# Kernel optimization log

Hardware: AMD Instinct MI355X
Metric: run time of the kernel (lower is better)

The kernel has to match this reference:

```python
import jax, jax.numpy as jnp
import numpy as np

V, BLK, D, H, L = 50257, 2048, 768, 12, 4
HD = D // H
EPS = 1e-5


def _ln(x, w, b):
    mu = jnp.mean(x, axis=-1, keepdims=True)
    var = jnp.mean(jnp.square(x - mu), axis=-1, keepdims=True)
    return (x - mu) * jax.lax.rsqrt(var + EPS) * w + b


def setup_inputs() -> dict:
    key = jax.random.key(0)
    ks = iter(jax.random.split(key, 32))
    s = 0.02
    idx = jax.random.randint(next(ks), (2, 2048), 0, V)
    inp = {
        "idx": idx,
        "wte": jax.random.normal(next(ks), (V, D), jnp.float32) * s,
        "wpe": jax.random.normal(next(ks), (BLK, D), jnp.float32) * s,
        # stacked per-layer params [L, ...]
        "ln1_w": jnp.ones((L, D), jnp.float32),
        "ln1_b": jnp.zeros((L, D), jnp.float32),
        "attn_w": jax.random.normal(next(ks), (L, D, 3 * D), jnp.float32) * s,
        "attn_b": jnp.zeros((L, 3 * D), jnp.float32),
        "proj_w": jax.random.normal(next(ks), (L, D, D), jnp.float32) * (s / np.sqrt(2 * L)),
        "proj_b": jnp.zeros((L, D), jnp.float32),
        "ln2_w": jnp.ones((L, D), jnp.float32),
        "ln2_b": jnp.zeros((L, D), jnp.float32),
        "fc_w": jax.random.normal(next(ks), (L, D, 4 * D), jnp.float32) * s,
        "fc_b": jnp.zeros((L, 4 * D), jnp.float32),
        "fcp_w": jax.random.normal(next(ks), (L, 4 * D, D), jnp.float32) * (s / np.sqrt(2 * L)),
        "fcp_b": jnp.zeros((L, D), jnp.float32),
        "lnf_w": jnp.ones((D,), jnp.float32),
        "lnf_b": jnp.zeros((D,), jnp.float32),
    }
    return inp


def _gpt_forward(idx, wte, wpe, ln1_w, ln1_b, attn_w, attn_b, proj_w, proj_b,
                 ln2_w, ln2_b, fc_w, fc_b, fcp_w, fcp_b, lnf_w, lnf_b):
    B, T = idx.shape
    x = wte[idx] + wpe[:T]  # [B,T,D]; dropout p=0 -> identity
    causal = jnp.tril(jnp.ones((T, T), bool))
    scale = 1.0 / np.sqrt(HD)

    def block(x, p):
        l1w, l1b, aw, ab, pw, pb, l2w, l2b, fw, fb, fpw, fpb = p
        h = _ln(x, l1w, l1b)
        qkv = h @ aw + ab  # [B,T,3D]
        q, k, v = jnp.split(qkv, 3, axis=-1)
        q = q.reshape(B, T, H, HD).transpose(0, 2, 1, 3)  # [B,H,T,hd]
        k = k.reshape(B, T, H, HD).transpose(0, 2, 1, 3)
        v = v.reshape(B, T, H, HD).transpose(0, 2, 1, 3)
        att = jnp.einsum('bhqd,bhkd->bhqk', q, k) * scale
        att = jnp.where(causal, att, -jnp.inf)
        att = jax.nn.softmax(att, axis=-1)
        y = jnp.einsum('bhqk,bhkd->bhqd', att, v)
        y = y.transpose(0, 2, 1, 3).reshape(B, T, D)
        x = x + y @ pw + pb
        h2 = _ln(x, l2w, l2b)
        m = jax.nn.gelu(h2 @ fw + fb, approximate=False) @ fpw + fpb
        return x + m, None

    params = (ln1_w, ln1_b, attn_w, attn_b, proj_w, proj_b,
              ln2_w, ln2_b, fc_w, fc_b, fcp_w, fcp_b)
    x, _ = jax.lax.scan(block, x, params)
    x = _ln(x, lnf_w, lnf_b)
    # inference path: logits only for last position, lm_head tied to wte
    logits = x[:, -1:, :] @ wte.T  # [B,1,V]
    return logits


def reference(idx, wte, wpe, ln1_w, ln1_b, attn_w, attn_b, proj_w, proj_b,
              ln2_w, ln2_b, fc_w, fc_b, fcp_w, fcp_b, lnf_w, lnf_b):
    return _gpt_forward(idx, wte, wpe, ln1_w, ln1_b, attn_w, attn_b, proj_w, proj_b,
                        ln2_w, ln2_b, fc_w, fc_b, fcp_w, fcp_b, lnf_w, lnf_b)
```

## Files before the change

### kernel.cpp

```cpp
#include <hip/hip_runtime.h>
#include <math.h>

#define V 50257
#define B 2
#define T 2048
#define D 768
#define H 12
#define HD 64
#define L 4
#define D3 (3*D)
#define D4 (4*D)
#define NTOK (B*T)
#define EPS 1e-5f

typedef __bf16 v8bf __attribute__((ext_vector_type(8)));
typedef __bf16 v4bf __attribute__((ext_vector_type(4)));
typedef unsigned short v8us __attribute__((ext_vector_type(8)));
typedef float  v4f  __attribute__((ext_vector_type(4)));

#define GAS(p) ((const __attribute__((address_space(1))) void*)(p))
#define LAS(p) ((__attribute__((address_space(3))) void*)(p))

#define LIDX(row, chunk) ((row)*64 + ((((chunk) ^ ((row)&7)))<<3))
#define C2IDX(row, chunk) ((row)*256 + ((((chunk) ^ (((row)&7)<<2)))<<3))

#define SBAR() asm volatile("s_barrier" ::: "memory")

__device__ __forceinline__ float gelu_fast(float x) {
    float z  = fabsf(x) * 0.70710678118f;
    float tt = 1.f / (1.f + 0.3275911f * z);
    float poly = tt * (0.254829592f + tt * (-0.284496736f + tt * (1.421413741f +
                 tt * (-1.453152027f + tt * 1.061405429f))));
    float er = 1.f - poly * __expf(-z * z);
    er = (x < 0.f) ? -er : er;
    return 0.5f * x * (1.f + er);
}

__global__ __launch_bounds__(256) void prep_kernel(
        const int* __restrict__ idx, const float* __restrict__ wte,
        const float* __restrict__ wpe, float* __restrict__ x,
        const float* __restrict__ aw_all,  const float* __restrict__ pw_all,
        const float* __restrict__ fw_all,  const float* __restrict__ fpw_all,
        __bf16* __restrict__ awt_all, __bf16* __restrict__ pwt_all,
        __bf16* __restrict__ fwt_all, __bf16* __restrict__ fpwt_all) {
    int bid = blockIdx.x;
    if (bid < 3072) {
        int e = (bid * 256 + threadIdx.x) * 4;
        int pos = e / D;
        int d   = e - pos * D;
        int t   = pos & (T - 1);
        int tok = idx[pos];
        const float4 a  = *(const float4*)(wte + (size_t)tok * D + d);
        const float4 p4 = *(const float4*)(wpe + (size_t)t * D + d);
        float4 r; r.x = a.x + p4.x; r.y = a.y + p4.y; r.z = a.z + p4.z; r.w = a.w + p4.w;
        *(float4*)(x + e) = r;
        return;
    }
    bid -= 3072;
    const int l = bid / 6912; bid -= l * 6912;
    const float* W; __bf16* Wt; int K, N, bx, by;
    if (bid < 1728)      {             W = aw_all  + (size_t)l * D  * D3; Wt = awt_all  + (size_t)l * D3 * D;  K = D;  N = D3; bx = bid % 72; by = bid / 72; }
    else if (bid < 2304) { bid -= 1728; W = pw_all  + (size_t)l * D  * D;  Wt = pwt_all  + (size_t)l * D  * D;  K = D;  N = D;  bx = bid % 24; by = bid / 24; }
    else if (bid < 4608) { bid -= 2304; W = fw_all  + (size_t)l * D  * D4; Wt = fwt_all  + (size_t)l * D4 * D;  K = D;  N = D4; bx = bid % 96; by = bid / 96; }
    else                 { bid -= 4608; W = fpw_all + (size_t)l * D4 * D;  Wt = fpwt_all + (size_t)l * D  * D4; K = D4; N = D;  bx = bid % 24; by = bid / 24; }
    __shared__ float t[32][33];
    const int n0 = bx * 32, k0 = by * 32;
    const int tx = threadIdx.x & 31, ty = threadIdx.x >> 5;
    #pragma unroll
    for (int p = 0; p < 4; ++p)
        t[ty + 8 * p][tx] = W[(size_t)(k0 + ty + 8 * p) * N + n0 + tx];
    __syncthreads();
    #pragma unroll
    for (int p = 0; p < 4; ++p)
        Wt[(size_t)(n0 + ty + 8 * p) * K + k0 + tx] = (__bf16)t[tx][ty + 8 * p];
}

__global__ __launch_bounds__(256) void ln_kernel(const float* __restrict__ X,
                                                 const float* __restrict__ w,
                                                 const float* __restrict__ b,
                                                 __bf16* __restrict__ Y,
                                                 int src_mul, int src_off) {
    int srow = blockIdx.x * src_mul + src_off;
    const float* xr = X + (size_t)srow * D;
    float v[3];
    float s = 0.f, s2 = 0.f;
    #pragma unroll
    for (int j = 0; j < 3; ++j) {
        v[j] = xr[threadIdx.x + 256 * j];
        s += v[j];
        s2 += v[j] * v[j];
    }
    #pragma unroll
    for (int off = 32; off; off >>= 1) {
        s  += __shfl_xor(s, off);
        s2 += __shfl_xor(s2, off);
    }
    __shared__ float ss[4], ss2[4];
    int wave = threadIdx.x >> 6, lane = threadIdx.x & 63;
    if (lane == 0) { ss[wave] = s; ss2[wave] = s2; }
    __syncthreads();
    s  = ss[0] + ss[1] + ss[2] + ss[3];
    s2 = ss2[0] + ss2[1] + ss2[2] + ss2[3];
    float mu  = s * (1.f / D);
    float var = s2 * (1.f / D) - mu * mu;
    float rs  = rsqrtf(var + EPS);
    __bf16* yr = Y + (size_t)blockIdx.x * D;
    #pragma unroll
    for (int j = 0; j < 3; ++j) {
        int c = threadIdx.x + 256 * j;
        yr[c] = (__bf16)((v[j] - mu) * rs * w[c] + b[c]);
    }
}

template<bool DOGELU>
__global__ __launch_bounds__(512) void gemm256(const __bf16* __restrict__ A,
                                               const __bf16* __restrict__ Wt,
                                               const float* __restrict__ bias,
                                               __bf16* __restrict__ Cout,
                                               int N, int K) {
    __shared__ __align__(16) __bf16 sm[32768];
    const int tid  = threadIdx.x;
    const int w    = tid >> 6;
    const int lane = tid & 63;
    const int wm   = w >> 2;
    const int wn   = w & 3;

    int fid = blockIdx.y * gridDim.x + blockIdx.x;
    const int nwg = gridDim.x * gridDim.y;
    fid = (fid & 7) * (nwg >> 3) + (fid >> 3);
    const int row0 = (fid / gridDim.x) * 256;
    const int col0 = (fid % gridDim.x) * 256;

    const int l15 = lane & 15;
    const int lq8 = (lane >> 4) * 8;
    const __bf16* gAsrc[2];
    const __bf16* gBsrc[2];
    {
        #pragma unroll
        for (int rep = 0; rep < 2; ++rep) {
            int ga = w * 2 + rep;
            int awm = ga >> 3, ai = ga & 7;
            gAsrc[rep] = A + (size_t)(row0 + awm * 128 + ai * 16 + l15) * K + lq8;
            int gb = w * 2 + rep;
            int bwn = gb >> 2, bj = gb & 3;
            gBsrc[rep] = Wt + (size_t)(col0 + bwn * 64 + bj * 16 + l15) * K + lq8;
        }
    }

    auto stage = [&](int bsel) {
        __bf16* dst = sm + bsel * 16384;
        #pragma unroll
        for (int rep = 0; rep < 2; ++rep) {
            const int g = w * 2 + rep;
            __builtin_amdgcn_global_load_lds(GAS(gAsrc[rep]), LAS(dst + (size_t)(g * 64 + lane) * 8), 16, 0, 0);
            __builtin_amdgcn_global_load_lds(GAS(gBsrc[rep]), LAS(dst + 8192 + (size_t)(g * 64 + lane) * 8), 16, 0, 0);
            gAsrc[rep] += 32; gBsrc[rep] += 32;
        }
    };

    const int nt = K >> 5;
    stage(0);

    v4f acc[8][4] = {};
    for (int t = 0; t < nt; ++t) {
        const int cb = (t & 1) * 16384;
        if (t + 1 < nt) {
            stage((t + 1) & 1);
            asm volatile("s_waitcnt vmcnt(4)\n\ts_barrier" ::: "memory");
        } else {
            asm volatile("s_waitcnt vmcnt(0)\n\ts_barrier" ::: "memory");
        }
        v8bf bf[4];
        #pragma unroll
        for (int j = 0; j < 4; ++j)
            bf[j] = *(const v8bf*)(sm + cb + 8192 + (size_t)((wn * 4 + j) * 64 + lane) * 8);
        #pragma unroll
        for (int i = 0; i < 8; ++i) {
            v8bf af = *(const v8bf*)(sm + cb + (size_t)((wm * 8 + i) * 64 + lane) * 8);
            #pragma unroll
            for (int j = 0; j < 4; ++j)
                acc[i][j] = __builtin_amdgcn_mfma_f32_16x16x32_bf16(af, bf[j], acc[i][j], 0, 0, 0);
        }
        SBAR();
    }

    const int er = (lane >> 4) * 4;
    const int ec = lane & 15;
    #pragma unroll
    for (int half = 0; half < 2; ++half) {
        if (wm == half) {
            #pragma unroll
            for (int j = 0; j < 4; ++j) {
                const int col = wn * 64 + j * 16 + ec;
                const float bval = bias[col0 + col];
                const int chunk = col >> 3, ce = col & 7;
                #pragma unroll
                for (int i = 0; i < 8; ++i) {
                    const int rowb = i * 16 + er;
                    #pragma unroll
                    for (int rr = 0; rr < 4; ++rr) {
                        float vv = acc[i][j][rr] + bval;
                        if (DOGELU) vv = gelu_fast(vv);
                        sm[C2IDX(rowb + rr, chunk) + ce] = (__bf16)vv;
                    }
                }
            }
        }
        __syncthreads();
        #pragma unroll
        for (int c = 0; c < 8; ++c) {
            const int chunkid = tid + c * 512;
            const int row = chunkid >> 5;
            const int cc  = chunkid & 31;
            *(v8us*)(void*)(Cout + (size_t)(row0 + half * 128 + row) * N + col0 + cc * 8) =
                *(const v8us*)(const void*)(sm + C2IDX(row, cc));
        }
        __syncthreads();
    }
}

__global__ __launch_bounds__(256) void gemm64(const __bf16* __restrict__ A,
                                              const __bf16* __restrict__ Wt,
                                              const float* __restrict__ bias,
                                              const float* __restrict__ res,
                                              float* __restrict__ Cout,
                                              int N, int K) {
    __shared__ __align__(16) __bf16 sm[24576];
    const int tid  = threadIdx.x;
    const int w    = tid >> 6;
    const int lane = tid & 63;

    int fid = blockIdx.y * gridDim.x + blockIdx.x;
    const int nwg = gridDim.x * gridDim.y;
    fid = (fid & 7) * (nwg >> 3) + (fid >> 3);
    const int row0 = (fid / gridDim.x) * 64;
    const int col0 = (fid % gridDim.x) * 64;

    const int srow = ((tid >> 7) & 3) * 16 + (tid & 15);
    const int sk   = ((tid >> 4) & 7) * 8;
    const __bf16* gA0 = A  + (size_t)(row0 + srow) * K + sk;
    const __bf16* gA1 = gA0 + (size_t)32 * K;
    const __bf16* gB0 = Wt + (size_t)(col0 + srow) * K + sk;
    const __bf16* gB1 = gB0 + (size_t)32 * K;

    auto stage = [&](int bsel) {
        __bf16* dst = sm + bsel * 8192;
        __builtin_amdgcn_global_load_lds(GAS(gA0), LAS(dst + (size_t)tid * 8), 16, 0, 0);
        __builtin_amdgcn_global_load_lds(GAS(gA1), LAS(dst + (size_t)(tid + 256) * 8), 16, 0, 0);
        __builtin_amdgcn_global_load_lds(GAS(gB0), LAS(dst + 4096 + (size_t)tid * 8), 16, 0, 0);
        __builtin_amdgcn_global_load_lds(GAS(gB1), LAS(dst + 4096 + (size_t)(tid + 256) * 8), 16, 0, 0);
        gA0 += 64; gA1 += 64; gB0 += 64; gB1 += 64;
    };

    const int wr = w >> 1, wc = w & 1;
    const __bf16* rA = sm + wr * 2048 + lane * 8;
    const __bf16* rB = sm + 4096 + wc * 2048 + lane * 8;

    const int nt = K >> 6;
    stage(0); stage(1);

    v4f acc[2][2] = {};
    for (int t = 0; t < nt; ++t) {
        const int cb = (t % 3) * 8192;
        if (t + 2 < nt) {
            stage((t + 2) % 3);
            asm volatile("s_waitcnt vmcnt(8)\n\ts_barrier" ::: "memory");
        } else if (t + 1 < nt) {
            asm volatile("s_waitcnt vmcnt(4)\n\ts_barrier" ::: "memory");
        } else {
            asm volatile("s_waitcnt vmcnt(0)\n\ts_barrier" ::: "memory");
        }
        #pragma unroll
        for (int h = 0; h < 2; ++h) {
            v8bf af[2], bfr[2];
            #pragma unroll
            for (int i = 0; i < 2; ++i) af[i]  = *(const v8bf*)(rA + cb + i * 1024 + h * 512);
            #pragma unroll
            for (int j = 0; j < 2; ++j) bfr[j] = *(const v8bf*)(rB + cb + j * 1024 + h * 512);
            #pragma unroll
            for (int i = 0; i < 2; ++i)
                #pragma unroll
                for (int j = 0; j < 2; ++j)
                    acc[i][j] = __builtin_amdgcn_mfma_f32_16x16x32_bf16(af[i], bfr[j], acc[i][j], 0, 0, 0);
        }
        SBAR();
    }

    float* smf = (float*)sm;
    const int er = (lane >> 4) * 4;
    const int ec = lane & 15;
    #pragma unroll
    for (int j = 0; j < 2; ++j) {
        const int col = wc * 32 + j * 16 + ec;
        const float bval = bias[col0 + col];
        #pragma unroll
        for (int i = 0; i < 2; ++i) {
            #pragma unroll
            for (int rr = 0; rr < 4; ++rr) {
                const int row = wr * 32 + i * 16 + er + rr;
                smf[row * 64 + (col ^ ((row & 3) << 4))] = acc[i][j][rr] + bval;
            }
        }
    }
    __syncthreads();
    #pragma unroll
    for (int c = 0; c < 4; ++c) {
        const int chunkid = tid + c * 256;
        const int row = chunkid >> 4;
        const int c0  = (chunkid & 15) * 4;
        float4 vv = *(const float4*)(smf + row * 64 + (c0 ^ ((row & 3) << 4)));
        const float4 rv = *(const float4*)(res + (size_t)(row0 + row) * N + col0 + c0);
        vv.x += rv.x; vv.y += rv.y; vv.z += rv.z; vv.w += rv.w;
        *(float4*)(Cout + (size_t)(row0 + row) * N + col0 + c0) = vv;
    }
}

__global__ __launch_bounds__(256) void attn_mfma(const __bf16* __restrict__ qkv,
                                                 __bf16* __restrict__ y) {
    __shared__ __align__(16) __bf16 Qs[4096];
    __shared__ __align__(16) __bf16 Ks[4096];
    __shared__ __align__(16) __bf16 Vt[4096];
    __shared__ __align__(16) __bf16 Ps[4][1024];

    const int tid  = threadIdx.x;
    const int w    = tid >> 6;
    const int lane = tid & 63;
    const int quad = lane >> 4;
    const int l4   = lane & 15;

    int fid = blockIdx.x;
    const int nwg = gridDim.x;
    fid = (fid & 7) * (nwg >> 3) + (fid >> 3);

    const int qt = 31 - (fid & 31);
    const int bh = fid >> 5;
    const int b  = bh / H;
    const int h  = bh - b * H;
    const int q0 = qt * 64;

    const __bf16* base = qkv + (size_t)(b * T) * D3 + h * HD;

    {
        int c = tid;
        #pragma unroll
        for (int rep = 0; rep < 2; ++rep, c += 256) {
            int row = c >> 3, ch = c & 7;
            v8us v = *(const v8us*)(const void*)(base + (size_t)(q0 + row) * D3 + ch * 8);
            *(v8us*)(void*)(Qs + LIDX(row, ch)) = v;
        }
    }

    const int krow = tid >> 3, kch = tid & 7;
    const int vkp = tid & 31, vdc = tid >> 5;
    const __bf16* kp0 = base + D     + (size_t)krow * D3 + kch * 8;
    const __bf16* kp1 = kp0 + (size_t)32 * D3;
    const __bf16* vp0 = base + 2 * D + (size_t)(2 * vkp) * D3 + vdc * 8;
    const __bf16* vp1 = vp0 + D3;

    v8us kr0 = *(const v8us*)(const void*)kp0;
    v8us kr1 = *(const v8us*)(const void*)kp1;
    v8us vr0 = *(const v8us*)(const void*)vp0;
    v8us vr1 = *(const v8us*)(const void*)vp1;

    float m_local = -INFINITY;
    v4f o[4] = {};
    v4f sacc = {};
    v8bf qf[2];
    v8bf vones;
    #pragma unroll
    for (int i = 0; i < 8; ++i) vones[i] = (__bf16)1.0f;

    const int nt = qt + 1;
    const size_t adv = (size_t)64 * D3;
    const int qrow = q0 + w * 16 + l4;

    for (int kt = 0; kt < nt; ++kt) {
        const int k0 = kt * 64;
        *(v8us*)(void*)(Ks + LIDX(krow, kch))      = kr0;
        *(v8us*)(void*)(Ks + LIDX(krow + 32, kch)) = kr1;
        #pragma unroll
        for (int j = 0; j < 8; ++j) {
            int dim = vdc * 8 + j;
            int idx = dim * 64 + ((((vkp >> 2) ^ (dim & 7))) << 3) + ((vkp & 3) << 1);
            *(unsigned int*)(void*)(Vt + idx) =
                ((unsigned int)vr1[j] << 16) | (unsigned int)vr0[j];
        }
        __syncthreads();

        if (kt == 0) {
            #pragma unroll
            for (int kh = 0; kh < 2; ++kh)
                qf[kh] = *(const v8bf*)(Qs + LIDX(w * 16 + l4, kh * 4 + quad));
        }
        if (kt + 1 < nt) {
            kp0 += adv; kp1 += adv; vp0 += adv; vp1 += adv;
            kr0 = *(const v8us*)(const void*)kp0;
            kr1 = *(const v8us*)(const void*)kp1;
            vr0 = *(const v8us*)(const void*)vp0;
            vr1 = *(const v8us*)(const void*)vp1;
        }

        v4f s[4] = {};
        __builtin_amdgcn_s_setprio(1);
        #pragma unroll
        for (int kh = 0; kh < 2; ++kh) {
            #pragma unroll
            for (int jb = 0; jb < 4; ++jb) {
                v8bf bk = *(const v8bf*)(Ks + LIDX(jb * 16 + l4, kh * 4 + quad));
                s[jb] = __builtin_amdgcn_mfma_f32_16x16x32_bf16(bk, qf[kh], s[jb], 0, 0, 0);
            }
        }
        __builtin_amdgcn_s_setprio(0);

        float sv[4][4];
        float mx = -INFINITY;
        #pragma unroll
        for (int jb = 0; jb < 4; ++jb) {
            #pragma unroll
            for (int rg = 0; rg < 4; ++rg) {
                float vvv = s[jb][rg] * 0.125f;
                if (k0 + jb * 16 + quad * 4 + rg > qrow) vvv = -INFINITY;
                sv[jb][rg] = vvv;
                mx = fmaxf(mx, vvv);
            }
        }
        mx = fmaxf(mx, __shfl_xor(mx, 16));
        mx = fmaxf(mx, __shfl_xor(mx, 32));
        if (!__all(mx <= m_local + 8.f)) {
            const float mnew    = fmaxf(m_local, mx);
            const float alpha_l = __expf(m_local - mnew);
            m_local = mnew;
            float a4[4];
            #pragma unroll
            for (int r = 0; r < 4; ++r) a4[r] = __shfl(alpha_l, quad * 4 + r);
            #pragma unroll
            for (int r = 0; r < 4; ++r) {
                sacc[r] *= a4[r];
                #pragma unroll
                for (int db = 0; db < 4; ++db) o[db][r] *= a4[r];
            }
        }
        #pragma unroll
        for (int jb = 0; jb < 4; ++jb) {
            v4bf pk;
            #pragma unroll
            for (int rg = 0; rg < 4; ++rg)
                pk[rg] = (__bf16)__expf(sv[jb][rg] - m_local);
            *(v4bf*)(void*)(&Ps[w][LIDX(l4, jb * 2 + (quad >> 1)) + ((quad & 1) << 2)]) = pk;
        }
        __builtin_amdgcn_s_setprio(1);
        #pragma unroll
        for (int kh = 0; kh < 2; ++kh) {
            v8bf ap = *(const v8bf*)(&Ps[w][LIDX(l4, kh * 4 + quad)]);
            sacc = __builtin_amdgcn_mfma_f32_16x16x32_bf16(ap, vones, sacc, 0, 0, 0);
            #pragma unroll
            for (int db = 0; db < 4; ++db) {
                v8bf bv = *(const v8bf*)(Vt + LIDX(db * 16 + l4, kh * 4 + quad));
                o[db] = __builtin_amdgcn_mfma_f32_16x16x32_bf16(ap, bv, o[db], 0, 0, 0);
            }
        }
        __builtin_amdgcn_s_setprio(0);
        __syncthreads();
    }

    #pragma unroll
    for (int db = 0; db < 4; ++db) {
        #pragma unroll
        for (int r = 0; r < 4; ++r) {
            const int q = q0 + w * 16 + quad * 4 + r;
            y[(size_t)(b * T + q) * D + h * HD + db * 16 + l4] =
                (__bf16)(o[db][r] / sacc[r]);
        }
    }
}

__global__ __launch_bounds__(256) void logits_kernel(const __bf16* __restrict__ xf,
                                                     const float* __restrict__ wte,
                                                     float* __restrict__ out) {
    int wave = threadIdx.x >> 6;
    int lane = threadIdx.x & 63;
    int v = blockIdx.x * 4 + wave;
    if (v >= V) return;
    const float4* wr = (const float4*)(wte + (size_t)v * D);
    const v4bf*   x0 = (const v4bf*)(xf);
    const v4bf*   x1 = (const v4bf*)(xf + D);
    float s0 = 0.f, s1 = 0.f;
    #pragma unroll
    for (int j = 0; j < 3; ++j) {
        float4 wv = wr[lane + 64 * j];
        v4bf a0 = x0[lane + 64 * j];
        v4bf a1 = x1[lane + 64 * j];
        s0 = fmaf(wv.x, (float)a0[0], s0); s0 = fmaf(wv.y, (float)a0[1], s0);
        s0 = fmaf(wv.z, (float)a0[2], s0); s0 = fmaf(wv.w, (float)a0[3], s0);
        s1 = fmaf(wv.x, (float)a1[0], s1); s1 = fmaf(wv.y, (float)a1[1], s1);
        s1 = fmaf(wv.z, (float)a1[2], s1); s1 = fmaf(wv.w, (float)a1[3], s1);
    }
    #pragma unroll
    for (int off = 32; off; off >>= 1) {
        s0 += __shfl_xor(s0, off);
        s1 += __shfl_xor(s1, off);
    }
    if (lane == 0) { out[v] = s0; out[V + v] = s1; }
}

extern "C" void kernel_launch(void* const* d_in, const int* in_sizes, int n_in,
                              void* d_out, int out_size, void* d_ws, size_t ws_size,
                              hipStream_t stream) {
    const int*   idx    = (const int*)  d_in[0];
    const float* wte    = (const float*)d_in[1];
    const float* wpe    = (const float*)d_in[2];
    const float* ln1_w  = (const float*)d_in[3];
    const float* ln1_b  = (const float*)d_in[4];
    const float* attn_w = (const float*)d_in[5];
    const float* attn_b = (const float*)d_in[6];
    const float* proj_w = (const float*)d_in[7];
    const float* proj_b = (const float*)d_in[8];
    const float* ln2_w  = (const float*)d_in[9];
    const float* ln2_b  = (const float*)d_in[10];
    const float* fc_w   = (const float*)d_in[11];
    const float* fc_b   = (const float*)d_in[12];
    const float* fcp_w  = (const float*)d_in[13];
    const float* fcp_b  = (const float*)d_in[14];
    const float* lnf_w  = (const float*)d_in[15];
    const float* lnf_b  = (const float*)d_in[16];
    float* out = (float*)d_out;

    char* ws = (char*)d_ws;
    float*  x    = (float*)ws;  ws += (size_t)NTOK * D  * 4;
    __bf16* qkvb = (__bf16*)ws;
    __bf16* gb   = (__bf16*)ws; ws += (size_t)NTOK * D4 * 2;
    __bf16* hb   = (__bf16*)ws; ws += (size_t)NTOK * D  * 2;
    __bf16* yb   = (__bf16*)ws; ws += (size_t)NTOK * D  * 2;
    __bf16* awt  = (__bf16*)ws; ws += (size_t)L * D3 * D   * 2;
    __bf16* pwt  = (__bf16*)ws; ws += (size_t)L * D  * D   * 2;
    __bf16* fwt  = (__bf16*)ws; ws += (size_t)L * D4 * D   * 2;
    __bf16* fpwt = (__bf16*)ws; ws += (size_t)L * D  * D4  * 2;
    __bf16* xf   = (__bf16*)ws; ws += (size_t)B * D    * 2;

    prep_kernel<<<3072 + 6912 * L, 256, 0, stream>>>(idx, wte, wpe, x,
                                                     attn_w, proj_w, fc_w, fcp_w,
                                                     awt, pwt, fwt, fpwt);

    for (int l = 0; l < L; ++l) {
        const float* l1w = ln1_w + l * D;
        const float* l1b = ln1_b + l * D;
        const float* ab  = attn_b + l * D3;
        const float* pb  = proj_b + l * D;
        const float* l2w = ln2_w + l * D;
        const float* l2b = ln2_b + l * D;
        const float* fb  = fc_b + l * D4;
        const float* fpb = fcp_b + l * D;
        const __bf16* awl  = awt  + (size_t)l * D3 * D;
        const __bf16* pwl  = pwt  + (size_t)l * D  * D;
        const __bf16* fwl  = fwt  + (size_t)l * D4 * D;
        const __bf16* fpwl = fpwt + (size_t)l * D  * D4;

        ln_kernel<<<NTOK, 256, 0, stream>>>(x, l1w, l1b, hb, 1, 0);
        gemm256<false><<<dim3(D3 / 256, NTOK / 256), 512, 0, stream>>>(
            hb, awl, ab, qkvb, D3, D);
        attn_mfma<<<B * H * (T / 64), 256, 0, stream>>>(qkvb, yb);
        gemm64<<<dim3(D / 64, NTOK / 64), 256, 0, stream>>>(
            yb, pwl, pb, x, x, D, D);
        ln_kernel<<<NTOK, 256, 0, stream>>>(x, l2w, l2b, hb, 1, 0);
        gemm256<true><<<dim3(D4 / 256, NTOK / 256), 512, 0, stream>>>(
            hb, fwl, fb, gb, D4, D);
        gemm64<<<dim3(D / 64, NTOK / 64), 256, 0, stream>>>(
            gb, fpwl, fpb, x, x, D, D4);
    }

    ln_kernel<<<B, 256, 0, stream>>>(x, lnf_w, lnf_b, xf, T, T - 1);
    logits_kernel<<<(V + 3) / 4, 256, 0, stream>>>(xf, wte, out);
}
```

Before: 1.280 ms.

## Deepen GEMM LDS pipeline with phased prefetch and double-buffer attention K/V

The 256x256 GEMM now works on 64-wide K tiles held in a 4-slot LDS buffer that is twice as large. Each iteration is split into eight phases that interleave half-tile global-to-LDS loads with MFMA bursts, using explicit barriers, waitcnt and sched_barrier. The attention kernel double-buffers its K and V shared tiles, so the next tile is written to LDS during the current tile's compute and one barrier per iteration is dropped. Both changes aim to hide global load latency behind matrix math, at the cost of more LDS, which may lower occupancy, and a tricky synchronisation scheme.

```diff
diff --git a/kernel.cpp b/kernel.cpp
--- a/kernel.cpp
+++ b/kernel.cpp
@@ -22,6 +22,7 @@
 #define LAS(p) ((__attribute__((address_space(3))) void*)(p))
 
 #define LIDX(row, chunk) ((row)*64 + ((((chunk) ^ ((row)&7)))<<3))
+#define CIDX(row, chunk) ((row)*128 + ((((chunk) ^ ((row)&7)))<<3))
 #define C2IDX(row, chunk) ((row)*256 + ((((chunk) ^ (((row)&7)<<2)))<<3))
 
 #define SBAR() asm volatile("s_barrier" ::: "memory")
@@ -112,18 +113,56 @@
     }
 }
 
+#define DS_A(BUF,KH,I) (*(const v8bf*)(sm + ((BUF)<<15) + ((KH)<<13) + ((wm*8+(I))<<9) + (lane<<3)))
+#define DS_B(BUF,KH,J) (*(const v8bf*)(sm + ((BUF)<<15) + 16384 + ((KH)<<13) + ((wn*4+(J))<<9) + (lane<<3)))
+
+#define MFMA_ROW(I, AV) \
+    acc[I][0] = __builtin_amdgcn_mfma_f32_16x16x32_bf16(AV, bfr[0], acc[I][0], 0, 0, 0); \
+    acc[I][1] = __builtin_amdgcn_mfma_f32_16x16x32_bf16(AV, bfr[1], acc[I][1], 0, 0, 0); \
+    acc[I][2] = __builtin_amdgcn_mfma_f32_16x16x32_bf16(AV, bfr[2], acc[I][2], 0, 0, 0); \
+    acc[I][3] = __builtin_amdgcn_mfma_f32_16x16x32_bf16(AV, bfr[3], acc[I][3], 0, 0, 0);
+
+#define PH_E(BUF, KH, SMAT, SKH, SKT) { \
+    bfr[0] = DS_B(BUF,KH,0); bfr[1] = DS_B(BUF,KH,1); \
+    bfr[2] = DS_B(BUF,KH,2); bfr[3] = DS_B(BUF,KH,3); \
+    v8bf a0 = DS_A(BUF,KH,0), a1 = DS_A(BUF,KH,1); \
+    v8bf a2 = DS_A(BUF,KH,2), a3 = DS_A(BUF,KH,3); \
+    stage_half(SMAT, SKH, SKT); \
+    __builtin_amdgcn_s_barrier(); \
+    asm volatile("s_waitcnt lgkmcnt(0)" ::: "memory"); \
+    __builtin_amdgcn_sched_barrier(0); \
+    __builtin_amdgcn_s_setprio(1); \
+    MFMA_ROW(0, a0) MFMA_ROW(1, a1) MFMA_ROW(2, a2) MFMA_ROW(3, a3) \
+    __builtin_amdgcn_s_setprio(0); \
+    __builtin_amdgcn_s_barrier(); }
+
+#define PH_O(BUF, KH, SMAT, SKH, SKT) { \
+    v8bf a4 = DS_A(BUF,KH,4), a5 = DS_A(BUF,KH,5); \
+    v8bf a6 = DS_A(BUF,KH,6), a7 = DS_A(BUF,KH,7); \
+    stage_half(SMAT, SKH, SKT); \
+    __builtin_amdgcn_s_barrier(); \
+    asm volatile("s_waitcnt lgkmcnt(0)" ::: "memory"); \
+    __builtin_amdgcn_sched_barrier(0); \
+    __builtin_amdgcn_s_setprio(1); \
+    MFMA_ROW(4, a4) MFMA_ROW(5, a5) MFMA_ROW(6, a6) MFMA_ROW(7, a7) \
+    __builtin_amdgcn_s_setprio(0); \
+    asm volatile("s_waitcnt vmcnt(8)" ::: "memory"); \
+    __builtin_amdgcn_s_barrier(); }
+
 template<bool DOGELU>
 __global__ __launch_bounds__(512) void gemm256(const __bf16* __restrict__ A,
                                                const __bf16* __restrict__ Wt,
                                                const float* __restrict__ bias,
                                                __bf16* __restrict__ Cout,
                                                int N, int K) {
-    __shared__ __align__(16) __bf16 sm[32768];
+    __shared__ __align__(16) __bf16 sm[65536];
     const int tid  = threadIdx.x;
     const int w    = tid >> 6;
     const int lane = tid & 63;
     const int wm   = w >> 2;
     const int wn   = w & 3;
+    const int l15  = lane & 15;
+    const int lq8  = (lane >> 4) * 8;
 
     int fid = blockIdx.y * gridDim.x + blockIdx.x;
     const int nwg = gridDim.x * gridDim.y;
@@ -131,58 +170,41 @@
     const int row0 = (fid / gridDim.x) * 256;
     const int col0 = (fid % gridDim.x) * 256;
 
-    const int l15 = lane & 15;
-    const int lq8 = (lane >> 4) * 8;
-    const __bf16* gAsrc[2];
-    const __bf16* gBsrc[2];
-    {
-        #pragma unroll
-        for (int rep = 0; rep < 2; ++rep) {
-            int ga = w * 2 + rep;
-            int awm = ga >> 3, ai = ga & 7;
-            gAsrc[rep] = A + (size_t)(row0 + awm * 128 + ai * 16 + l15) * K + lq8;
-            int gb = w * 2 + rep;
-            int bwn = gb >> 2, bj = gb & 3;
-            gBsrc[rep] = Wt + (size_t)(col0 + bwn * 64 + bj * 16 + l15) * K + lq8;
-        }
-    }
-
-    auto stage = [&](int bsel) {
-        __bf16* dst = sm + bsel * 16384;
-        #pragma unroll
-        for (int rep = 0; rep < 2; ++rep) {
-            const int g = w * 2 + rep;
-            __builtin_amdgcn_global_load_lds(GAS(gAsrc[rep]), LAS(dst + (size_t)(g * 64 + lane) * 8), 16, 0, 0);
-            __builtin_amdgcn_global_load_lds(GAS(gBsrc[rep]), LAS(dst + 8192 + (size_t)(g * 64 + lane) * 8), 16, 0, 0);
-            gAsrc[rep] += 32; gBsrc[rep] += 32;
-        }
+    const int nt = K >> 6;
+    const __bf16* const Ab = A  + (size_t)(row0 + w * 16 + l15) * K + lq8;
+    const __bf16* const Bb = Wt + (size_t)(col0 + w * 16 + l15) * K + lq8;
+
+    auto stage_half = [&](int mat, int kh, int kt) {
+        const int kts  = kt < nt ? kt : nt - 1;
+        const int koff = kts * 64 + kh * 32;
+        __bf16* dst = sm + ((kt & 1) << 15) + (mat << 14) + (kh << 13) + (w << 9) + (lane << 3);
+        const __bf16* s = (mat ? Bb : Ab) + koff;
+        __builtin_amdgcn_global_load_lds(GAS(s), LAS(dst), 16, 0, 0);
+        __builtin_amdgcn_global_load_lds(GAS(s + (size_t)128 * K), LAS(dst + 4096), 16, 0, 0);
     };
 
-    const int nt = K >> 5;
-    stage(0);
+    stage_half(0, 0, 0); stage_half(1, 0, 0);
+    stage_half(0, 1, 0); stage_half(1, 1, 0);
+    stage_half(0, 0, 1); stage_half(1, 0, 1);
+    asm volatile("s_waitcnt vmcnt(8)" ::: "memory");
+    __builtin_amdgcn_s_barrier();
 
     v4f acc[8][4] = {};
-    for (int t = 0; t < nt; ++t) {
-        const int cb = (t & 1) * 16384;
-        if (t + 1 < nt) {
-            stage((t + 1) & 1);
-            asm volatile("s_waitcnt vmcnt(4)\n\ts_barrier" ::: "memory");
-        } else {
-            asm volatile("s_waitcnt vmcnt(0)\n\ts_barrier" ::: "memory");
-        }
-        v8bf bf[4];
-        #pragma unroll
-        for (int j = 0; j < 4; ++j)
-            bf[j] = *(const v8bf*)(sm + cb + 8192 + (size_t)((wn * 4 + j) * 64 + lane) * 8);
-        #pragma unroll
-        for (int i = 0; i < 8; ++i) {
-            v8bf af = *(const v8bf*)(sm + cb + (size_t)((wm * 8 + i) * 64 + lane) * 8);
-            #pragma unroll
-            for (int j = 0; j < 4; ++j)
-                acc[i][j] = __builtin_amdgcn_mfma_f32_16x16x32_bf16(af, bf[j], acc[i][j], 0, 0, 0);
-        }
-        SBAR();
-    }
+    v8bf bfr[4];
+    const int niter = nt >> 1;
+    for (int it = 0; it < niter; ++it) {
+        const int t0 = 2 * it, t1 = t0 + 1;
+        PH_E(0, 0,  0, 1, t1)
+        PH_O(0, 0,  1, 1, t1)
+        PH_E(0, 1,  0, 0, t0 + 2)
+        PH_O(0, 1,  1, 0, t0 + 2)
+        PH_E(1, 0,  0, 1, t0 + 2)
+        PH_O(1, 0,  1, 1, t0 + 2)
+        PH_E(1, 1,  0, 0, t0 + 3)
+        PH_O(1, 1,  1, 0, t0 + 3)
+    }
+    asm volatile("s_waitcnt vmcnt(0)" ::: "memory");
+    __syncthreads();
 
     const int er = (lane >> 4) * 4;
     const int ec = lane & 15;
@@ -318,8 +340,8 @@
 __global__ __launch_bounds__(256) void attn_mfma(const __bf16* __restrict__ qkv,
                                                  __bf16* __restrict__ y) {
     __shared__ __align__(16) __bf16 Qs[4096];
-    __shared__ __align__(16) __bf16 Ks[4096];
-    __shared__ __align__(16) __bf16 Vt[4096];
+    __shared__ __align__(16) __bf16 Ks[8192];
+    __shared__ __align__(16) __bf16 Vt[8192];
     __shared__ __align__(16) __bf16 Ps[4][1024];
 
     const int tid  = threadIdx.x;
@@ -362,43 +384,45 @@
     v8us vr0 = *(const v8us*)(const void*)vp0;
     v8us vr1 = *(const v8us*)(const void*)vp1;
 
+    const int nt = qt + 1;
+    const size_t adv = (size_t)64 * D3;
+
+    *(v8us*)(void*)(Ks + LIDX(krow, kch))      = kr0;
+    *(v8us*)(void*)(Ks + LIDX(krow + 32, kch)) = kr1;
+    #pragma unroll
+    for (int j = 0; j < 8; ++j) {
+        int dim = vdc * 8 + j;
+        int idx = dim * 64 + ((((vkp >> 2) ^ (dim & 7))) << 3) + ((vkp & 3) << 1);
+        *(unsigned int*)(void*)(Vt + idx) =
+            ((unsigned int)vr1[j] << 16) | (unsigned int)vr0[j];
+    }
+    if (nt > 1) {
+        kp0 += adv; kp1 += adv; vp0 += adv; vp1 += adv;
+        kr0 = *(const v8us*)(const void*)kp0;
+        kr1 = *(const v8us*)(const void*)kp1;
+        vr0 = *(const v8us*)(const void*)vp0;
+        vr1 = *(const v8us*)(const void*)vp1;
+    }
+    __syncthreads();
+
+    v8bf qf[2];
+    #pragma unroll
+    for (int kh = 0; kh < 2; ++kh)
+        qf[kh] = *(const v8bf*)(Qs + LIDX(w * 16 + l4, kh * 4 + quad));
+
     float m_local = -INFINITY;
     v4f o[4] = {};
     v4f sacc = {};
-    v8bf qf[2];
     v8bf vones;
     #pragma unroll
     for (int i = 0; i < 8; ++i) vones[i] = (__bf16)1.0f;
 
-    const int nt = qt + 1;
-    const size_t adv = (size_t)64 * D3;
     const int qrow = q0 + w * 16 + l4;
 
     for (int kt = 0; kt < nt; ++kt) {
+        const int cur = (kt & 1) << 12;
+        const int nxt = cur ^ 4096;
         const int k0 = kt * 64;
-        *(v8us*)(void*)(Ks + LIDX(krow, kch))      = kr0;
-        *(v8us*)(void*)(Ks + LIDX(krow + 32, kch)) = kr1;
-        #pragma unroll
-        for (int j = 0; j < 8; ++j) {
-            int dim = vdc * 8 + j;
-            int idx = dim * 64 + ((((vkp >> 2) ^ (dim & 7))) << 3) + ((vkp & 3) << 1);
-            *(unsigned int*)(void*)(Vt + idx) =
-                ((unsigned int)vr1[j] << 16) | (unsigned int)vr0[j];
-        }
-        __syncthreads();
-
-        if (kt == 0) {
-            #pragma unroll
-            for (int kh = 0; kh < 2; ++kh)
-                qf[kh] = *(const v8bf*)(Qs + LIDX(w * 16 + l4, kh * 4 + quad));
-        }
-        if (kt + 1 < nt) {
-            kp0 += adv; kp1 += adv; vp0 += adv; vp1 += adv;
-            kr0 = *(const v8us*)(const void*)kp0;
-            kr1 = *(const v8us*)(const void*)kp1;
-            vr0 = *(const v8us*)(const void*)vp0;
-            vr1 = *(const v8us*)(const void*)vp1;
-        }
 
         v4f s[4] = {};
         __builtin_amdgcn_s_setprio(1);
@@ -406,11 +430,30 @@
         for (int kh = 0; kh < 2; ++kh) {
             #pragma unroll
             for (int jb = 0; jb < 4; ++jb) {
-                v8bf bk = *(const v8bf*)(Ks + LIDX(jb * 16 + l4, kh * 4 + quad));
+                v8bf bk = *(const v8bf*)(Ks + cur + LIDX(jb * 16 + l4, kh * 4 + quad));
                 s[jb] = __builtin_amdgcn_mfma_f32_16x16x32_bf16(bk, qf[kh], s[jb], 0, 0, 0);
             }
         }
         __builtin_amdgcn_s_setprio(0);
+
+        if (kt + 1 < nt) {
+            *(v8us*)(void*)(Ks + nxt + LIDX(krow, kch))      = kr0;
+            *(v8us*)(void*)(Ks + nxt + LIDX(krow + 32, kch)) = kr1;
+            #pragma unroll
+            for (int j = 0; j < 8; ++j) {
+                int dim = vdc * 8 + j;
+                int idx = dim * 64 + ((((vkp >> 2) ^ (dim & 7))) << 3) + ((vkp & 3) << 1);
+                *(unsigned int*)(void*)(Vt + nxt + idx) =
+                    ((unsigned int)vr1[j] << 16) | (unsigned int)vr0[j];
+            }
+            if (kt + 2 < nt) {
+                kp0 += adv; kp1 += adv; vp0 += adv; vp1 += adv;
+                kr0 = *(const v8us*)(const void*)kp0;
+                kr1 = *(const v8us*)(const void*)kp1;
+                vr0 = *(const v8us*)(const void*)vp0;
+                vr1 = *(const v8us*)(const void*)vp1;
+            }
+        }
 
         float sv[4][4];
         float mx = -INFINITY;
@@ -455,12 +498,12 @@
             sacc = __builtin_amdgcn_mfma_f32_16x16x32_bf16(ap, vones, sacc, 0, 0, 0);
             #pragma unroll
             for (int db = 0; db < 4; ++db) {
-                v8bf bv = *(const v8bf*)(Vt + LIDX(db * 16 + l4, kh * 4 + quad));
+                v8bf bv = *(const v8bf*)(Vt + cur + LIDX(db * 16 + l4, kh * 4 + quad));
                 o[db] = __builtin_amdgcn_mfma_f32_16x16x32_bf16(ap, bv, o[db], 0, 0, 0);
             }
         }
         __builtin_amdgcn_s_setprio(0);
-        __syncthreads();
+        if (kt + 1 < nt) __syncthreads();
     }
 
     #pragma unroll
```

New measurement: 1.273 ms. About the same (-0.6%).
